# Kernel optimization log

Hardware: AMD Instinct MI355X
Metric: run time of the kernel (lower is better)

## Reference

```python
import jax, jax.numpy as jnp
import numpy as np
from jax import lax

LN_EPS = 1e-6  # flax LayerNorm default


def _layernorm(x, scale, bias):
    mu = jnp.mean(x, axis=-1, keepdims=True)
    var = jnp.mean(jnp.square(x - mu), axis=-1, keepdims=True)
    return (x - mu) * lax.rsqrt(var + LN_EPS) * scale + bias


def _lstm_layer(c0, h0, Wi, Wh, b, x):
    # x: [B, T, F]; carry c/h: [B, H]; gate order i, f, g, o (flax)
    def step(carry, xt):
        c, h = carry
        z = xt @ Wi + h @ Wh + b  # [B, 4H]
        i, f, g, o = jnp.split(z, 4, axis=-1)
        i = jax.nn.sigmoid(i); f = jax.nn.sigmoid(f)
        g = jnp.tanh(g); o = jax.nn.sigmoid(o)
        c = f * c + i * g
        h = o * jnp.tanh(c)
        return (c, h), h
    (cT, hT), hs = lax.scan(step, (c0, h0), jnp.swapaxes(x, 0, 1))
    return cT, hT, jnp.swapaxes(hs, 0, 1)  # hs: [B, T, H]


def setup_inputs() -> dict:
    key = jax.random.key(0)
    ks = jax.random.split(key, 16)
    B, T, F, H, P, A = 64, 128, 512, 1024, 1024, 32
    s = 0.05
    return {
        "x": jax.random.normal(ks[0], (B, T, F), jnp.float32),
        "c0": jnp.zeros((2, B, H), jnp.float32),
        "h0": jnp.zeros((2, B, H), jnp.float32),
        "W_pre": jax.random.normal(ks[1], (F, P), jnp.float32) * s,
        "b_pre": jnp.zeros((P,), jnp.float32),
        "ln_scale": jnp.ones((P,), jnp.float32),
        "ln_bias": jnp.zeros((P,), jnp.float32),
        "Wi0": jax.random.normal(ks[2], (P, 4 * H), jnp.float32) * s,
        "Wh0": jax.random.normal(ks[3], (H, 4 * H), jnp.float32) * s,
        "b0": jnp.zeros((4 * H,), jnp.float32),
        "Wi1": jax.random.normal(ks[4], (H, 4 * H), jnp.float32) * s,
        "Wh1": jax.random.normal(ks[5], (H, 4 * H), jnp.float32) * s,
        "b1": jnp.zeros((4 * H,), jnp.float32),
        "W_post": jax.random.normal(ks[6], (H, P), jnp.float32) * s,
        "b_post": jnp.zeros((P,), jnp.float32),
        "W_out": jax.random.normal(ks[7], (P, A), jnp.float32) * s,
        "b_out": jnp.zeros((A,), jnp.float32),
        "training": False,
    }


def reference(x, c0, h0, W_pre, b_pre, ln_scale, ln_bias,
              Wi0, Wh0, b0, Wi1, Wh1, b1,
              W_post, b_post, W_out, b_out, training):
    # preprocessing: Dense -> LayerNorm -> relu
    h = jax.nn.relu(_layernorm(x @ W_pre + b_pre, ln_scale, ln_bias))
    # two stacked LSTM layers scanned over time
    c1, h1, h = _lstm_layer(c0[0], h0[0], Wi0, Wh0, b0, h)
    c2, h2, h = _lstm_layer(c0[1], h0[1], Wi1, Wh1, b1, h)
    # postprocessing: Dense -> relu (dropout deterministic => identity)
    h = jax.nn.relu(h @ W_post + b_post)
    logits = h @ W_out + b_out  # [B, T, action_dim]
    new_carry = (jnp.stack([c1, c2]), jnp.stack([h1, h2]))
    return new_carry, logits
```

## Files before the change

kernel.cpp:

```cpp
#include <hip/hip_runtime.h>
#include <hip/hip_bf16.h>
#include <math.h>

typedef __attribute__((ext_vector_type(8))) short short8;
typedef __attribute__((ext_vector_type(4))) float f32x4;
typedef __attribute__((ext_vector_type(4))) unsigned u32x4;
typedef unsigned short u16;
typedef unsigned long long u64;

__device__ __forceinline__ u16 f2bf(float f) {
    union { float f; unsigned u; } v; v.f = f;
    unsigned r = v.u + 0x7fffu + ((v.u >> 16) & 1u);
    return (u16)(r >> 16);
}
__device__ __forceinline__ float bf2f(u16 b) {
    union { unsigned u; float f; } v; v.u = ((unsigned)b) << 16;
    return v.f;
}
__device__ __forceinline__ float fast_sigmoid(float x) {
    return __builtin_amdgcn_rcpf(1.f + __expf(-x));
}
__device__ __forceinline__ float fast_tanh(float x) {
    return 1.f - 2.f * __builtin_amdgcn_rcpf(1.f + __expf(2.f * x));
}
__device__ __forceinline__ u32x4 ldg16(const void* p) {
    u32x4 r;
    asm volatile("global_load_dwordx4 %0, %1, off"
                 : "=v"(r) : "v"(p) : "memory");
    return r;
}

__device__ __forceinline__ void tr_tile(const float* __restrict__ W,
                                        u16* __restrict__ WT, int K, int N,
                                        int bid, int tid, float (*tile)[33]) {
    int gx = N >> 5;
    int bx = bid % gx, by = bid / gx;
    int n0 = bx * 32, k0 = by * 32;
    int tx = tid & 31, ty = tid >> 5;
    #pragma unroll
    for (int j = 0; j < 32; j += 8)
        tile[ty + j][tx] = W[(size_t)(k0 + ty + j) * N + n0 + tx];
    __syncthreads();
    #pragma unroll
    for (int j = 0; j < 32; j += 8)
        WT[(size_t)(n0 + ty + j) * K + k0 + tx] = f2bf(tile[tx][ty + j]);
}

__global__ __launch_bounds__(256) void k_prep(
    const float* __restrict__ x, u16* __restrict__ Xb,
    const float* __restrict__ h0, u16* __restrict__ hs0, u16* __restrict__ hs1,
    unsigned* __restrict__ ctr,
    const float* __restrict__ Wpre, u16* __restrict__ WTpre,
    const float* __restrict__ Wi0, u16* __restrict__ WTi0,
    const float* __restrict__ Wh0, u16* __restrict__ WTh0,
    const float* __restrict__ Wi1, u16* __restrict__ WTi1,
    const float* __restrict__ Wh1, u16* __restrict__ WTh1,
    const float* __restrict__ Wpost, u16* __restrict__ WTpost,
    const float* __restrict__ Wout, u16* __restrict__ WTout) {
    __shared__ float tile[32][33];
    int bid = blockIdx.x, tid = threadIdx.x;
    if (bid == 0) {
        for (int i = tid; i < 4096; i += 256) ctr[i] = 0u;
        return;
    }
    bid -= 1;
    if (bid < 16384) {
        int i = bid * 256 + tid;
        Xb[i] = f2bf(x[i]);
        return;
    }
    bid -= 16384;
    if (bid < 512) {
        int i = bid * 256 + tid;
        int layer = i >> 16, j = i & 65535;
        int b = j >> 10, jj = j & 1023;
        u16 v = f2bf(h0[(size_t)layer * 65536 + j]);
        u16* dst = layer ? hs1 : hs0;
        dst[(size_t)(jj >> 3) * 512 + b * 8 + (jj & 7)] = v;
        return;
    }
    bid -= 512;
    if (bid < 512)  { tr_tile(Wpre,  WTpre,  512,  1024, bid, tid, tile); return; }
    bid -= 512;
    if (bid < 4096) { tr_tile(Wi0,   WTi0,   1024, 4096, bid, tid, tile); return; }
    bid -= 4096;
    if (bid < 4096) { tr_tile(Wh0,   WTh0,   1024, 4096, bid, tid, tile); return; }
    bid -= 4096;
    if (bid < 4096) { tr_tile(Wi1,   WTi1,   1024, 4096, bid, tid, tile); return; }
    bid -= 4096;
    if (bid < 4096) { tr_tile(Wh1,   WTh1,   1024, 4096, bid, tid, tile); return; }
    bid -= 4096;
    if (bid < 1024) { tr_tile(Wpost, WTpost, 1024, 1024, bid, tid, tile); return; }
    bid -= 1024;
    tr_tile(Wout, WTout, 1024, 32, bid, tid, tile);
}
#define PREP_BLOCKS (1 + 16384 + 512 + 512 + 4 * 4096 + 1024 + 32)

template <int MODE>
__global__ __launch_bounds__(256) void k_gemm(const u16* __restrict__ A,
                                              const u16* __restrict__ BT,
                                              const float* __restrict__ bias,
                                              void* __restrict__ Cout,
                                              int M, int N, int K) {
    const int w = threadIdx.x >> 6, l = threadIdx.x & 63;
    const int lm = l & 15, lq = l >> 4;
    const int r0 = blockIdx.y * 64 + w * 16;
    const int c0 = blockIdx.x * 64;
    const u16* arow = A + (size_t)(r0 + lm) * K + lq * 8;
    const u16* bp0 = BT + (size_t)(c0 + lm) * K + lq * 8;
    const u16* bp1 = bp0 + (size_t)16 * K;
    const u16* bp2 = bp0 + (size_t)32 * K;
    const u16* bp3 = bp0 + (size_t)48 * K;
    f32x4 acc0 = {0.f, 0.f, 0.f, 0.f}, acc1 = acc0, acc2 = acc0, acc3 = acc0;
    for (int k0 = 0; k0 < K; k0 += 32) {
        short8 a = *(const short8*)(arow + k0);
        acc0 = __builtin_amdgcn_mfma_f32_16x16x32_bf16(a, *(const short8*)(bp0 + k0), acc0, 0, 0, 0);
        acc1 = __builtin_amdgcn_mfma_f32_16x16x32_bf16(a, *(const short8*)(bp1 + k0), acc1, 0, 0, 0);
        acc2 = __builtin_amdgcn_mfma_f32_16x16x32_bf16(a, *(const short8*)(bp2 + k0), acc2, 0, 0, 0);
        acc3 = __builtin_amdgcn_mfma_f32_16x16x32_bf16(a, *(const short8*)(bp3 + k0), acc3, 0, 0, 0);
    }
    f32x4 accs[4] = {acc0, acc1, acc2, acc3};
    #pragma unroll
    for (int nt = 0; nt < 4; nt++) {
        #pragma unroll
        for (int r = 0; r < 4; r++) {
            int row = r0 + lq * 4 + r;
            int col = c0 + nt * 16 + lm;
            float v = accs[nt][r] + bias[col];
            if (MODE == 0) {
                ((float*)Cout)[(size_t)row * N + col] = v;
            } else {
                if (MODE == 2) v = fmaxf(v, 0.f);
                ((u16*)Cout)[(size_t)row * N + col] = f2bf(v);
            }
        }
    }
}

__global__ __launch_bounds__(256) void k_ln_relu(const float* __restrict__ X,
                                                 const float* __restrict__ scale,
                                                 const float* __restrict__ bias,
                                                 u16* __restrict__ preS) {
    const int N = 1024;
    int row = blockIdx.x;
    int b = row >> 7, t = row & 127;
    const float* x = X + (size_t)row * N;
    __shared__ float vbuf[1024];
    float s = 0.f, ss = 0.f;
    float vals[4];
    #pragma unroll
    for (int j = 0; j < 4; j++) {
        float v = x[threadIdx.x + 256 * j];
        vals[j] = v; s += v; ss += v * v;
    }
    #pragma unroll
    for (int o = 32; o > 0; o >>= 1) { s += __shfl_down(s, o); ss += __shfl_down(ss, o); }
    __shared__ float rs[4], rss[4];
    int w = threadIdx.x >> 6;
    if ((threadIdx.x & 63) == 0) { rs[w] = s; rss[w] = ss; }
    __syncthreads();
    __shared__ float smu, sinv;
    if (threadIdx.x == 0) {
        float a = rs[0] + rs[1] + rs[2] + rs[3];
        float bq = rss[0] + rss[1] + rss[2] + rss[3];
        float mu = a * (1.f / N);
        float var = bq * (1.f / N) - mu * mu;
        smu = mu; sinv = rsqrtf(var + 1e-6f);
    }
    __syncthreads();
    float mu = smu, inv = sinv;
    #pragma unroll
    for (int j = 0; j < 4; j++) {
        int i = threadIdx.x + 256 * j;
        float v = (vals[j] - mu) * inv * scale[i] + bias[i];
        vbuf[i] = fmaxf(v, 0.f);
    }
    __syncthreads();
    if (threadIdx.x < 128) {
        int g = threadIdx.x;
        union { u16 h[8]; u32x4 v; } pk;
        #pragma unroll
        for (int e = 0; e < 8; e++) pk.h[e] = f2bf(vbuf[g * 8 + e]);
        *(u32x4*)(preS + (size_t)t * 65536 + (size_t)g * 512 + b * 8) = pk.v;
    }
}

#define FBLOCKS 256
__global__ __launch_bounds__(512, 1) void k_lstm_fused(
    const u16* __restrict__ WiT0, const u16* __restrict__ WhT0,
    const u16* __restrict__ WiT1, const u16* __restrict__ WhT1,
    const u16* __restrict__ preS, const float* __restrict__ b0v,
    const float* __restrict__ b1v, const float* __restrict__ c0_all,
    u16* __restrict__ hs0, u16* __restrict__ hs1, u16* __restrict__ Hp,
    float* __restrict__ out, unsigned* __restrict__ ctr) {
    const int bk = blockIdx.x;
    const int role = bk >> 7;
    const int bkl = bk & 127;
    const int tid = threadIdx.x;
    const int w = tid >> 6, l = tid & 63, lm = l & 15, lq = l >> 4;
    const int kp = w >> 2, rt = w & 3;

    __shared__ u16 whs[65536];
    __shared__ float zbuf[2 * 64 * 33];
    __shared__ int gflag[2];

    {
        const u16* Wx = role ? WiT1 : WiT0;
        const u16* Wh = role ? WhT1 : WhT0;
        for (int f = tid; f < 8192; f += 512) {
            int flm = f & 15, flq = (f >> 4) & 3;
            int fi = (f >> 6) & 31;
            int rest = f >> 11;
            int fg = rest & 1, fkp = (rest >> 1) & 1;
            int lc = fg * 16 + flm;
            int gcolw = (lc >> 3) * 1024 + bkl * 8 + (lc & 7);
            int k = fi * 32 + flq * 8;
            const u16* src = (fkp == 0 ? Wx : Wh) + (size_t)gcolw * 1024 + k;
            *(short8*)(whs + (size_t)f * 8) = *(const short8*)src;
        }
    }
    if (tid == 0) { gflag[0] = -1; gflag[1] = -1; }
    const int u = tid & 7, b = tid >> 3;
    const int gcol = bkl * 8 + u;
    float c = (c0_all + (size_t)role * 65536)[(size_t)b * 1024 + gcol];
    const float* bv = role ? b1v : b0v;
    float bi0 = bv[gcol], bi1 = bv[1024 + gcol];
    float bi2 = bv[2048 + gcol], bi3 = bv[3072 + gcol];
    u16* hs_my = role ? hs1 : hs0;
    float* c_out = out + (size_t)role * 65536;
    float* h_out = out + 131072 + (size_t)role * 65536;
    const int lanoff = (lq * 16 + lm) * 8;
    __syncthreads();

    for (int t = 0; t < 128; t++) {
        if (role || kp == 1) {
            int need = (role && kp == 0) ? t + 1 : t;
            if (rt == 0) {
                if (need > 0) {
                    int cbase = (role && kp) ? 128 : 0;
                    for (;;) {
                        unsigned a0 = __hip_atomic_load(&ctr[(cbase + l) * 16], __ATOMIC_RELAXED,
                                                        __HIP_MEMORY_SCOPE_AGENT);
                        unsigned a1 = __hip_atomic_load(&ctr[(cbase + 64 + l) * 16], __ATOMIC_RELAXED,
                                                        __HIP_MEMORY_SCOPE_AGENT);
                        if (__all((a0 >= (unsigned)need) && (a1 >= (unsigned)need))) break;
                        __builtin_amdgcn_s_sleep(1);
                    }
                }
                __hip_atomic_store(&gflag[kp], need, __ATOMIC_RELAXED,
                                   __HIP_MEMORY_SCOPE_WORKGROUP);
            } else {
                while (__hip_atomic_load(&gflag[kp], __ATOMIC_RELAXED,
                                         __HIP_MEMORY_SCOPE_WORKGROUP) < need)
                    __builtin_amdgcn_s_sleep(1);
            }
        }

        const u16* abase;
        if (!role) abase = (kp == 0) ? preS + (size_t)t * 65536
                                     : hs0 + (size_t)t * 65536;
        else       abase = (kp == 0) ? hs0 + (size_t)(t + 1) * 65536
                                     : hs1 + (size_t)t * 65536;
        const u16* arow = abase + (size_t)lq * 512 + (rt * 16 + lm) * 8;
        const u16* bw0 = whs + kp * 32768 + lanoff;

        f32x4 zv = {0.f, 0.f, 0.f, 0.f};
        f32x4 ac0[4] = {zv, zv, zv, zv}, ac1[4] = {zv, zv, zv, zv};
        #define STEPF(Ai, i)                                                      \
        {   union { u32x4 q; short8 v; } _a; _a.q = (Ai);                         \
            short8 _b0 = *(const short8*)(bw0 + (i) * 512);                       \
            short8 _b1 = *(const short8*)(bw0 + 16384 + (i) * 512);               \
            ac0[(i) & 3] = __builtin_amdgcn_mfma_f32_16x16x32_bf16(_a.v, _b0, ac0[(i) & 3], 0, 0, 0); \
            ac1[(i) & 3] = __builtin_amdgcn_mfma_f32_16x16x32_bf16(_a.v, _b1, ac1[(i) & 3], 0, 0, 0); }

        u32x4 A0 = ldg16(arow +     0), A1 = ldg16(arow +  2048);
        u32x4 A2 = ldg16(arow +  4096), A3 = ldg16(arow +  6144);
        u32x4 A4 = ldg16(arow +  8192), A5 = ldg16(arow + 10240);
        u32x4 A6 = ldg16(arow + 12288), A7 = ldg16(arow + 14336);
        u32x4 A8 = ldg16(arow + 16384), A9 = ldg16(arow + 18432);
        u32x4 A10 = ldg16(arow + 20480), A11 = ldg16(arow + 22528);
        u32x4 A12 = ldg16(arow + 24576), A13 = ldg16(arow + 26624);
        u32x4 A14 = ldg16(arow + 28672), A15 = ldg16(arow + 30720);
        u32x4 A16 = ldg16(arow + 32768), A17 = ldg16(arow + 34816);
        u32x4 A18 = ldg16(arow + 36864), A19 = ldg16(arow + 38912);
        u32x4 A20 = ldg16(arow + 40960), A21 = ldg16(arow + 43008);
        u32x4 A22 = ldg16(arow + 45056), A23 = ldg16(arow + 47104);
        u32x4 A24 = ldg16(arow + 49152), A25 = ldg16(arow + 51200);
        u32x4 A26 = ldg16(arow + 53248), A27 = ldg16(arow + 55296);
        u32x4 A28 = ldg16(arow + 57344), A29 = ldg16(arow + 59392);
        u32x4 A30 = ldg16(arow + 61440), A31 = ldg16(arow + 63488);
        asm volatile("s_waitcnt vmcnt(24)"
                     : "+v"(A0), "+v"(A1), "+v"(A2), "+v"(A3),
                       "+v"(A4), "+v"(A5), "+v"(A6), "+v"(A7) :: "memory");
        STEPF(A0, 0) STEPF(A1, 1) STEPF(A2, 2) STEPF(A3, 3)
        STEPF(A4, 4) STEPF(A5, 5) STEPF(A6, 6) STEPF(A7, 7)
        asm volatile("s_waitcnt vmcnt(16)"
                     : "+v"(A8), "+v"(A9), "+v"(A10), "+v"(A11),
                       "+v"(A12), "+v"(A13), "+v"(A14), "+v"(A15) :: "memory");
        STEPF(A8, 8) STEPF(A9, 9) STEPF(A10, 10) STEPF(A11, 11)
        STEPF(A12, 12) STEPF(A13, 13) STEPF(A14, 14) STEPF(A15, 15)
        asm volatile("s_waitcnt vmcnt(8)"
                     : "+v"(A16), "+v"(A17), "+v"(A18), "+v"(A19),
                       "+v"(A20), "+v"(A21), "+v"(A22), "+v"(A23) :: "memory");
        STEPF(A16, 16) STEPF(A17, 17) STEPF(A18, 18) STEPF(A19, 19)
        STEPF(A20, 20) STEPF(A21, 21) STEPF(A22, 22) STEPF(A23, 23)
        asm volatile("s_waitcnt vmcnt(0)"
                     : "+v"(A24), "+v"(A25), "+v"(A26), "+v"(A27),
                       "+v"(A28), "+v"(A29), "+v"(A30), "+v"(A31) :: "memory");
        STEPF(A24, 24) STEPF(A25, 25) STEPF(A26, 26) STEPF(A27, 27)
        STEPF(A28, 28) STEPF(A29, 29) STEPF(A30, 30) STEPF(A31, 31)
        #undef STEPF
        f32x4 acc0 = (ac0[0] + ac0[1]) + (ac0[2] + ac0[3]);
        f32x4 acc1 = (ac1[0] + ac1[1]) + (ac1[2] + ac1[3]);

        {
            float* zb = zbuf + (size_t)kp * 2112;
            #pragma unroll
            for (int r = 0; r < 4; r++) {
                int row = rt * 16 + lq * 4 + r;
                zb[row * 33 + lm] = acc0[r];
                zb[row * 33 + 16 + lm] = acc1[r];
            }
        }
        __syncthreads();

        {
            const float* z0 = zbuf + (size_t)b * 33;
            const float* z1 = z0 + 2112;
            float gi = z0[u]      + z1[u]      + bi0;
            float gf = z0[8 + u]  + z1[8 + u]  + bi1;
            float gg = z0[16 + u] + z1[16 + u] + bi2;
            float go = z0[24 + u] + z1[24 + u] + bi3;
            gi = fast_sigmoid(gi);
            gf = fast_sigmoid(gf);
            gg = fast_tanh(gg);
            go = fast_sigmoid(go);
            c = gf * c + gi * gg;
            float h = go * fast_tanh(c);
            unsigned hv = (unsigned)f2bf(h);
            int base = l & 56;
            unsigned p0 = __shfl(hv, base + 0, 64) | (__shfl(hv, base + 1, 64) << 16);
            unsigned p1 = __shfl(hv, base + 2, 64) | (__shfl(hv, base + 3, 64) << 16);
            unsigned p2 = __shfl(hv, base + 4, 64) | (__shfl(hv, base + 5, 64) << 16);
            unsigned p3 = __shfl(hv, base + 6, 64) | (__shfl(hv, base + 7, 64) << 16);
            if (u == 0) {
                u32x4 pv = {p0, p1, p2, p3};
                u16* dst = hs_my + (size_t)(t + 1) * 65536 + (size_t)bkl * 512 + b * 8;
                asm volatile("global_store_dwordx4 %0, %1, off sc0 sc1"
                             :: "v"(dst), "v"(pv) : "memory");
                if (role) {
                    u16* d2 = Hp + (size_t)(t * 64 + b) * 1024 + bkl * 8;
                    *(u32x4*)d2 = pv;
                }
            }
            if (t == 127) {
                c_out[(size_t)b * 1024 + gcol] = c;
                h_out[(size_t)b * 1024 + gcol] = h;
            }
        }
        __syncthreads();

        if (tid == 0)
            __hip_atomic_store(&ctr[bk * 16], (unsigned)(t + 1), __ATOMIC_RELAXED,
                               __HIP_MEMORY_SCOPE_AGENT);
    }
}

__global__ __launch_bounds__(256) void k_logits(const u16* __restrict__ Pact,
                                                const u16* __restrict__ WoT,
                                                const float* __restrict__ bout,
                                                float* __restrict__ out) {
    int r = blockIdx.x * 8 + (threadIdx.x >> 5);
    int n = threadIdx.x & 31;
    const u16* a = Pact + (size_t)r * 1024;
    const u16* wv = WoT + (size_t)n * 1024;
    float s = 0.f;
    for (int k = 0; k < 1024; k += 8) {
        short8 av = *(const short8*)(a + k);
        short8 wvv = *(const short8*)(wv + k);
        #pragma unroll
        for (int j = 0; j < 8; j++)
            s += bf2f((u16)av[j]) * bf2f((u16)wvv[j]);
    }
    int t = r >> 6, b = r & 63;
    out[((size_t)b * 128 + t) * 32 + n] = s + bout[n];
}

extern "C" void kernel_launch(void* const* d_in, const int* in_sizes, int n_in,
                              void* d_out, int out_size, void* d_ws, size_t ws_size,
                              hipStream_t stream) {
    const float* x      = (const float*)d_in[0];
    const float* c0     = (const float*)d_in[1];
    const float* h0     = (const float*)d_in[2];
    const float* W_pre  = (const float*)d_in[3];
    const float* b_pre  = (const float*)d_in[4];
    const float* ln_s   = (const float*)d_in[5];
    const float* ln_b   = (const float*)d_in[6];
    const float* Wi0    = (const float*)d_in[7];
    const float* Wh0    = (const float*)d_in[8];
    const float* b0     = (const float*)d_in[9];
    const float* Wi1    = (const float*)d_in[10];
    const float* Wh1    = (const float*)d_in[11];
    const float* b1     = (const float*)d_in[12];
    const float* W_post = (const float*)d_in[13];
    const float* b_post = (const float*)d_in[14];
    const float* W_out  = (const float*)d_in[15];
    const float* b_out  = (const float*)d_in[16];
    float* out = (float*)d_out;

    char* ws = (char*)d_ws;
    size_t off = 0;
    auto alloc = [&](size_t bytes) {
        void* p = ws + off;
        off += (bytes + 255) & ~(size_t)255;
        return p;
    };
    u16* WTpre  = (u16*)alloc((size_t)1024 * 512 * 2);
    u16* WTi0   = (u16*)alloc((size_t)4096 * 1024 * 2);
    u16* WTh0   = (u16*)alloc((size_t)4096 * 1024 * 2);
    u16* WTi1   = (u16*)alloc((size_t)4096 * 1024 * 2);
    u16* WTh1   = (u16*)alloc((size_t)4096 * 1024 * 2);
    u16* WTpost = (u16*)alloc((size_t)1024 * 1024 * 2);
    u16* WTout  = (u16*)alloc((size_t)32 * 1024 * 2);
    u16* Xb     = (u16*)alloc((size_t)8192 * 512 * 2);
    u16* preS   = (u16*)alloc((size_t)128 * 65536 * 2);
    u16* hs0    = (u16*)alloc((size_t)129 * 65536 * 2);
    u16* hs1    = (u16*)alloc((size_t)129 * 65536 * 2);
    u16* postact= (u16*)alloc((size_t)8192 * 1024 * 2);
    unsigned* ctr = (unsigned*)alloc(32768);
    void* unionreg = alloc((size_t)8192 * 4096 * 2);
    float* pre_f32 = (float*)unionreg;
    u16* Hplain = (u16*)unionreg;

    k_prep<<<PREP_BLOCKS, 256, 0, stream>>>(
        x, Xb, h0, hs0, hs1, ctr,
        W_pre, WTpre, Wi0, WTi0, Wh0, WTh0, Wi1, WTi1, Wh1, WTh1,
        W_post, WTpost, W_out, WTout);

    k_gemm<0><<<dim3(16, 128), 256, 0, stream>>>(Xb, WTpre, b_pre, pre_f32, 8192, 1024, 512);
    k_ln_relu<<<8192, 256, 0, stream>>>(pre_f32, ln_s, ln_b, preS);

    {
        const u16* WiT0_ = WTi0; const u16* WhT0_ = WTh0;
        const u16* WiT1_ = WTi1; const u16* WhT1_ = WTh1;
        const u16* preS_ = preS; const float* b0_ = b0; const float* b1_ = b1;
        const float* c0_ = c0; u16* hs0_ = hs0; u16* hs1_ = hs1;
        u16* Hp_ = Hplain; float* out_ = out; unsigned* ctr_ = ctr;
        void* args[] = {&WiT0_, &WhT0_, &WiT1_, &WhT1_, &preS_, &b0_, &b1_,
                        &c0_, &hs0_, &hs1_, &Hp_, &out_, &ctr_};
        hipLaunchCooperativeKernel((void*)k_lstm_fused, dim3(FBLOCKS), dim3(512),
                                   args, 0, stream);
    }

    k_gemm<2><<<dim3(16, 128), 256, 0, stream>>>(Hplain, WTpost, b_post, postact,
                                                 8192, 1024, 1024);
    k_logits<<<1024, 256, 0, stream>>>(postact, WTout, b_out, out + 262144);
}
```

Before: 1.102 ms.

## Split K across warp groups so independent input half overlaps recurrent dependency wait

Each warp group now covers half of the K range for both the input projection and the recurrent term, instead of one group doing input and the other recurrent. Each wave first computes the part that needs no synchronization (input for layer 0, own recurrent state for layer 1) and only then polls the dependency counters, prefetched with an uncached load, before loading the dependent operand. This replaces the per-workgroup LDS flag handoff with a per-wave global counter check and hides sync latency behind MFMA work. It drops the 4-way accumulator split, which lengthens each MFMA dependency chain, and changes the zbuf padding.

```diff
diff --git a/kernel.cpp b/kernel.cpp
--- a/kernel.cpp
+++ b/kernel.cpp
@@ -26,6 +26,12 @@
 __device__ __forceinline__ u32x4 ldg16(const void* p) {
     u32x4 r;
     asm volatile("global_load_dwordx4 %0, %1, off"
+                 : "=v"(r) : "v"(p) : "memory");
+    return r;
+}
+__device__ __forceinline__ unsigned ldg_ctr(const unsigned* p) {
+    unsigned r;
+    asm volatile("global_load_dword %0, %1, off sc0 sc1"
                  : "=v"(r) : "v"(p) : "memory");
     return r;
 }
@@ -198,11 +204,10 @@
     const int bkl = bk & 127;
     const int tid = threadIdx.x;
     const int w = tid >> 6, l = tid & 63, lm = l & 15, lq = l >> 4;
-    const int kp = w >> 2, rt = w & 3;
+    const int grp = w >> 2, rt = w & 3;
 
     __shared__ u16 whs[65536];
-    __shared__ float zbuf[2 * 64 * 33];
-    __shared__ int gflag[2];
+    __shared__ float zbuf[2 * 64 * 34];
 
     {
         const u16* Wx = role ? WiT1 : WiT0;
@@ -219,7 +224,6 @@
             *(short8*)(whs + (size_t)f * 8) = *(const short8*)src;
         }
     }
-    if (tid == 0) { gflag[0] = -1; gflag[1] = -1; }
     const int u = tid & 7, b = tid >> 3;
     const int gcol = bkl * 8 + u;
     float c = (c0_all + (size_t)role * 65536)[(size_t)b * 1024 + gcol];
@@ -230,103 +234,119 @@
     float* c_out = out + (size_t)role * 65536;
     float* h_out = out + 131072 + (size_t)role * 65536;
     const int lanoff = (lq * 16 + lm) * 8;
+    const u16* bx0 = whs + grp * 8192 + lanoff;
+    const u16* bx1 = bx0 + 16384;
+    const u16* bh0 = whs + 32768 + grp * 8192 + lanoff;
+    const u16* bh1 = bh0 + 16384;
+    const u16* bS0 = role ? bh0 : bx0; const u16* bS1 = role ? bh1 : bx1;
+    const u16* bD0 = role ? bx0 : bh0; const u16* bD1 = role ? bx1 : bh1;
+    const int aoff = grp * 32768 + lq * 512 + (rt * 16 + lm) * 8;
     __syncthreads();
 
     for (int t = 0; t < 128; t++) {
-        if (role || kp == 1) {
-            int need = (role && kp == 0) ? t + 1 : t;
-            if (rt == 0) {
-                if (need > 0) {
-                    int cbase = (role && kp) ? 128 : 0;
-                    for (;;) {
-                        unsigned a0 = __hip_atomic_load(&ctr[(cbase + l) * 16], __ATOMIC_RELAXED,
-                                                        __HIP_MEMORY_SCOPE_AGENT);
-                        unsigned a1 = __hip_atomic_load(&ctr[(cbase + 64 + l) * 16], __ATOMIC_RELAXED,
-                                                        __HIP_MEMORY_SCOPE_AGENT);
-                        if (__all((a0 >= (unsigned)need) && (a1 >= (unsigned)need))) break;
-                        __builtin_amdgcn_s_sleep(1);
-                    }
+        if (role && t > 0) {
+            for (;;) {
+                unsigned a0 = __hip_atomic_load(&ctr[(128 + l) * 16], __ATOMIC_RELAXED,
+                                                __HIP_MEMORY_SCOPE_AGENT);
+                unsigned a1 = __hip_atomic_load(&ctr[(192 + l) * 16], __ATOMIC_RELAXED,
+                                                __HIP_MEMORY_SCOPE_AGENT);
+                if (__all((a0 >= (unsigned)t) && (a1 >= (unsigned)t))) break;
+                __builtin_amdgcn_s_sleep(1);
+            }
+        }
+        unsigned e0 = ldg_ctr(ctr + (size_t)l * 16);
+        unsigned e1 = ldg_ctr(ctr + (size_t)(64 + l) * 16);
+
+        const u16* sb = role ? hs1 + (size_t)t * 65536 : preS + (size_t)t * 65536;
+        const u16* db = role ? hs0 + (size_t)(t + 1) * 65536 : hs0 + (size_t)t * 65536;
+        const u16* arS = sb + aoff;
+        const u16* arD = db + aoff;
+
+        f32x4 acc0 = {0.f, 0.f, 0.f, 0.f}, acc1 = acc0;
+        #define STEPF(Ai, i, Bp0, Bp1)                                            \
+        {   union { u32x4 q; short8 v; } _a; _a.q = (Ai);                         \
+            short8 _b0 = *(const short8*)((Bp0) + (i) * 512);                     \
+            short8 _b1 = *(const short8*)((Bp1) + (i) * 512);                     \
+            acc0 = __builtin_amdgcn_mfma_f32_16x16x32_bf16(_a.v, _b0, acc0, 0, 0, 0); \
+            acc1 = __builtin_amdgcn_mfma_f32_16x16x32_bf16(_a.v, _b1, acc1, 0, 0, 0); }
+
+        u32x4 S0 = ldg16(arS +     0), S1 = ldg16(arS +  2048);
+        u32x4 S2 = ldg16(arS +  4096), S3 = ldg16(arS +  6144);
+        u32x4 S4 = ldg16(arS +  8192), S5 = ldg16(arS + 10240);
+        u32x4 S6 = ldg16(arS + 12288), S7 = ldg16(arS + 14336);
+        u32x4 S8 = ldg16(arS + 16384), S9 = ldg16(arS + 18432);
+        u32x4 S10 = ldg16(arS + 20480), S11 = ldg16(arS + 22528);
+        u32x4 S12 = ldg16(arS + 24576), S13 = ldg16(arS + 26624);
+        u32x4 S14 = ldg16(arS + 28672), S15 = ldg16(arS + 30720);
+        asm volatile("s_waitcnt vmcnt(8)"
+                     : "+v"(e0), "+v"(e1),
+                       "+v"(S0), "+v"(S1), "+v"(S2), "+v"(S3),
+                       "+v"(S4), "+v"(S5), "+v"(S6), "+v"(S7) :: "memory");
+        STEPF(S0, 0, bS0, bS1) STEPF(S1, 1, bS0, bS1)
+        STEPF(S2, 2, bS0, bS1) STEPF(S3, 3, bS0, bS1)
+        STEPF(S4, 4, bS0, bS1) STEPF(S5, 5, bS0, bS1)
+        STEPF(S6, 6, bS0, bS1) STEPF(S7, 7, bS0, bS1)
+        asm volatile("s_waitcnt vmcnt(0)"
+                     : "+v"(S8), "+v"(S9), "+v"(S10), "+v"(S11),
+                       "+v"(S12), "+v"(S13), "+v"(S14), "+v"(S15) :: "memory");
+        STEPF(S8, 8, bS0, bS1) STEPF(S9, 9, bS0, bS1)
+        STEPF(S10, 10, bS0, bS1) STEPF(S11, 11, bS0, bS1)
+        STEPF(S12, 12, bS0, bS1) STEPF(S13, 13, bS0, bS1)
+        STEPF(S14, 14, bS0, bS1) STEPF(S15, 15, bS0, bS1)
+
+        {
+            unsigned need = (unsigned)(role ? t + 1 : t);
+            if (need > 0 &&
+                !__all((int)((e0 >= need) && (e1 >= need)))) {
+                for (;;) {
+                    unsigned a0 = __hip_atomic_load(&ctr[l * 16], __ATOMIC_RELAXED,
+                                                    __HIP_MEMORY_SCOPE_AGENT);
+                    unsigned a1 = __hip_atomic_load(&ctr[(64 + l) * 16], __ATOMIC_RELAXED,
+                                                    __HIP_MEMORY_SCOPE_AGENT);
+                    if (__all((a0 >= need) && (a1 >= need))) break;
+                    __builtin_amdgcn_s_sleep(1);
                 }
-                __hip_atomic_store(&gflag[kp], need, __ATOMIC_RELAXED,
-                                   __HIP_MEMORY_SCOPE_WORKGROUP);
-            } else {
-                while (__hip_atomic_load(&gflag[kp], __ATOMIC_RELAXED,
-                                         __HIP_MEMORY_SCOPE_WORKGROUP) < need)
-                    __builtin_amdgcn_s_sleep(1);
-            }
-        }
-
-        const u16* abase;
-        if (!role) abase = (kp == 0) ? preS + (size_t)t * 65536
-                                     : hs0 + (size_t)t * 65536;
-        else       abase = (kp == 0) ? hs0 + (size_t)(t + 1) * 65536
-                                     : hs1 + (size_t)t * 65536;
-        const u16* arow = abase + (size_t)lq * 512 + (rt * 16 + lm) * 8;
-        const u16* bw0 = whs + kp * 32768 + lanoff;
-
-        f32x4 zv = {0.f, 0.f, 0.f, 0.f};
-        f32x4 ac0[4] = {zv, zv, zv, zv}, ac1[4] = {zv, zv, zv, zv};
-        #define STEPF(Ai, i)                                                      \
-        {   union { u32x4 q; short8 v; } _a; _a.q = (Ai);                         \
-            short8 _b0 = *(const short8*)(bw0 + (i) * 512);                       \
-            short8 _b1 = *(const short8*)(bw0 + 16384 + (i) * 512);               \
-            ac0[(i) & 3] = __builtin_amdgcn_mfma_f32_16x16x32_bf16(_a.v, _b0, ac0[(i) & 3], 0, 0, 0); \
-            ac1[(i) & 3] = __builtin_amdgcn_mfma_f32_16x16x32_bf16(_a.v, _b1, ac1[(i) & 3], 0, 0, 0); }
-
-        u32x4 A0 = ldg16(arow +     0), A1 = ldg16(arow +  2048);
-        u32x4 A2 = ldg16(arow +  4096), A3 = ldg16(arow +  6144);
-        u32x4 A4 = ldg16(arow +  8192), A5 = ldg16(arow + 10240);
-        u32x4 A6 = ldg16(arow + 12288), A7 = ldg16(arow + 14336);
-        u32x4 A8 = ldg16(arow + 16384), A9 = ldg16(arow + 18432);
-        u32x4 A10 = ldg16(arow + 20480), A11 = ldg16(arow + 22528);
-        u32x4 A12 = ldg16(arow + 24576), A13 = ldg16(arow + 26624);
-        u32x4 A14 = ldg16(arow + 28672), A15 = ldg16(arow + 30720);
-        u32x4 A16 = ldg16(arow + 32768), A17 = ldg16(arow + 34816);
-        u32x4 A18 = ldg16(arow + 36864), A19 = ldg16(arow + 38912);
-        u32x4 A20 = ldg16(arow + 40960), A21 = ldg16(arow + 43008);
-        u32x4 A22 = ldg16(arow + 45056), A23 = ldg16(arow + 47104);
-        u32x4 A24 = ldg16(arow + 49152), A25 = ldg16(arow + 51200);
-        u32x4 A26 = ldg16(arow + 53248), A27 = ldg16(arow + 55296);
-        u32x4 A28 = ldg16(arow + 57344), A29 = ldg16(arow + 59392);
-        u32x4 A30 = ldg16(arow + 61440), A31 = ldg16(arow + 63488);
-        asm volatile("s_waitcnt vmcnt(24)"
-                     : "+v"(A0), "+v"(A1), "+v"(A2), "+v"(A3),
-                       "+v"(A4), "+v"(A5), "+v"(A6), "+v"(A7) :: "memory");
-        STEPF(A0, 0) STEPF(A1, 1) STEPF(A2, 2) STEPF(A3, 3)
-        STEPF(A4, 4) STEPF(A5, 5) STEPF(A6, 6) STEPF(A7, 7)
-        asm volatile("s_waitcnt vmcnt(16)"
-                     : "+v"(A8), "+v"(A9), "+v"(A10), "+v"(A11),
-                       "+v"(A12), "+v"(A13), "+v"(A14), "+v"(A15) :: "memory");
-        STEPF(A8, 8) STEPF(A9, 9) STEPF(A10, 10) STEPF(A11, 11)
-        STEPF(A12, 12) STEPF(A13, 13) STEPF(A14, 14) STEPF(A15, 15)
+            }
+        }
+
+        u32x4 D0 = ldg16(arD +     0), D1 = ldg16(arD +  2048);
+        u32x4 D2 = ldg16(arD +  4096), D3 = ldg16(arD +  6144);
+        u32x4 D4 = ldg16(arD +  8192), D5 = ldg16(arD + 10240);
+        u32x4 D6 = ldg16(arD + 12288), D7 = ldg16(arD + 14336);
+        u32x4 D8 = ldg16(arD + 16384), D9 = ldg16(arD + 18432);
+        u32x4 D10 = ldg16(arD + 20480), D11 = ldg16(arD + 22528);
+        u32x4 D12 = ldg16(arD + 24576), D13 = ldg16(arD + 26624);
+        u32x4 D14 = ldg16(arD + 28672), D15 = ldg16(arD + 30720);
         asm volatile("s_waitcnt vmcnt(8)"
-                     : "+v"(A16), "+v"(A17), "+v"(A18), "+v"(A19),
-                       "+v"(A20), "+v"(A21), "+v"(A22), "+v"(A23) :: "memory");
-        STEPF(A16, 16) STEPF(A17, 17) STEPF(A18, 18) STEPF(A19, 19)
-        STEPF(A20, 20) STEPF(A21, 21) STEPF(A22, 22) STEPF(A23, 23)
+                     : "+v"(D0), "+v"(D1), "+v"(D2), "+v"(D3),
+                       "+v"(D4), "+v"(D5), "+v"(D6), "+v"(D7) :: "memory");
+        STEPF(D0, 0, bD0, bD1) STEPF(D1, 1, bD0, bD1)
+        STEPF(D2, 2, bD0, bD1) STEPF(D3, 3, bD0, bD1)
+        STEPF(D4, 4, bD0, bD1) STEPF(D5, 5, bD0, bD1)
+        STEPF(D6, 6, bD0, bD1) STEPF(D7, 7, bD0, bD1)
         asm volatile("s_waitcnt vmcnt(0)"
-                     : "+v"(A24), "+v"(A25), "+v"(A26), "+v"(A27),
-                       "+v"(A28), "+v"(A29), "+v"(A30), "+v"(A31) :: "memory");
-        STEPF(A24, 24) STEPF(A25, 25) STEPF(A26, 26) STEPF(A27, 27)
-        STEPF(A28, 28) STEPF(A29, 29) STEPF(A30, 30) STEPF(A31, 31)
+                     : "+v"(D8), "+v"(D9), "+v"(D10), "+v"(D11),
+                       "+v"(D12), "+v"(D13), "+v"(D14), "+v"(D15) :: "memory");
+        STEPF(D8, 8, bD0, bD1) STEPF(D9, 9, bD0, bD1)
+        STEPF(D10, 10, bD0, bD1) STEPF(D11, 11, bD0, bD1)
+        STEPF(D12, 12, bD0, bD1) STEPF(D13, 13, bD0, bD1)
+        STEPF(D14, 14, bD0, bD1) STEPF(D15, 15, bD0, bD1)
         #undef STEPF
-        f32x4 acc0 = (ac0[0] + ac0[1]) + (ac0[2] + ac0[3]);
-        f32x4 acc1 = (ac1[0] + ac1[1]) + (ac1[2] + ac1[3]);
 
         {
-            float* zb = zbuf + (size_t)kp * 2112;
+            float* zb = zbuf + (size_t)grp * 2176;
             #pragma unroll
             for (int r = 0; r < 4; r++) {
                 int row = rt * 16 + lq * 4 + r;
-                zb[row * 33 + lm] = acc0[r];
-                zb[row * 33 + 16 + lm] = acc1[r];
+                zb[row * 34 + lm] = acc0[r];
+                zb[row * 34 + 16 + lm] = acc1[r];
             }
         }
         __syncthreads();
 
         {
-            const float* z0 = zbuf + (size_t)b * 33;
-            const float* z1 = z0 + 2112;
+            const float* z0 = zbuf + (size_t)b * 34;
+            const float* z1 = z0 + 2176;
             float gi = z0[u]      + z1[u]      + bi0;
             float gf = z0[8 + u]  + z1[8 + u]  + bi1;
             float gg = z0[16 + u] + z1[16 + u] + bi2;
```

After: 1.208 ms. 9.7% more time.
